# Kernel optimization log

Hardware: AMD Instinct MI355X
Metric: run time of the kernel (lower is better)

## Reference

```python
import jax, jax.numpy as jnp
import numpy as np
import math

B, N, G, H, D = 16, 10000, 100, 128, 2
TANH_CLIP = 10.0
NEG_BIG = -1e8


def setup_inputs() -> dict:
    key = jax.random.key(0)
    ks = jax.random.split(key, 8)
    embeddings = jax.random.normal(ks[0], (B, N, H), dtype=jnp.float32)
    coordinates = jax.random.uniform(ks[1], (B, N, D), dtype=jnp.float32)
    last_node = jax.random.randint(ks[2], (B, G), 0, N)
    # group_ninf_mask: -inf where node already visited, 0 otherwise
    visited = jax.random.bernoulli(ks[3], 0.3, (B, G, N))
    group_ninf_mask = jnp.where(visited, -jnp.inf, 0.0).astype(jnp.float32)
    s = 1.0 / math.sqrt(H)
    Wq_graph_w = jax.random.normal(ks[4], (H, H), dtype=jnp.float32) * s
    Wq_first_w = jax.random.normal(ks[5], (H, H), dtype=jnp.float32) * s
    Wq_last_w = jax.random.normal(ks[6], (H, H), dtype=jnp.float32) * s
    W_visited_w = jax.random.normal(ks[7], (H, H), dtype=jnp.float32) * s
    return {
        "embeddings": embeddings,
        "coordinates": coordinates,
        "last_node": last_node,
        "group_ninf_mask": group_ninf_mask,
        "Wq_graph_w": Wq_graph_w,
        "Wq_first_w": Wq_first_w,
        "Wq_last_w": Wq_last_w,
        "W_visited_w": W_visited_w,
        "S": 0,
    }


def reference(embeddings, coordinates, last_node, group_ninf_mask,
              Wq_graph_w, Wq_first_w, Wq_last_w, W_visited_w, S):
    # --- state built in reset() ---
    # q_graph: Wq_graph(mean over nodes) -> [B,1,H]
    q_graph = jnp.einsum("bnh,oh->bno", jnp.mean(embeddings, axis=1, keepdims=True), Wq_graph_w)
    # logit_k is embeddings^T (multi_pointer == 1 path)

    # --- forward step ---
    # gather last-node embedding: [B,G,H]
    last_emb = jnp.take_along_axis(embeddings, last_node[:, :, None], axis=1)
    q_last = jnp.einsum("bgh,oh->bgo", last_emb, Wq_last_w)
    # q_first is None at the first step -> computed from the same last node
    q_first = jnp.einsum("bgh,oh->bgo", last_emb, Wq_first_w)

    # visited aggregation: mask with -inf -> 1.0, then bmm with embeddings / N
    mask_visited = jnp.where(jnp.isneginf(group_ninf_mask), 1.0, group_ninf_mask)
    agg = jnp.einsum("bgn,bnh->bgh", mask_visited, embeddings) / N
    q_visited = jnp.einsum("bgh,oh->bgo", agg, W_visited_w)

    # distances from last node to every node: cdist -> [B,G,N]
    last_coord = jnp.take_along_axis(coordinates, last_node[:, :, None], axis=1)  # [B,G,D]
    diff = last_coord[:, :, None, :] - coordinates[:, None, :, :]  # [B,G,N,D]
    distances = jnp.sqrt(jnp.maximum(jnp.sum(diff * diff, axis=-1), 1e-12))

    final_q = q_last + q_first + q_graph + q_visited  # add_more_query=True
    score = jnp.einsum("bgh,bnh->bgn", final_q, embeddings) / math.sqrt(H) \
            - distances / math.sqrt(2.0)
    score_clipped = TANH_CLIP * jnp.tanh(score)
    mask_prob = jnp.where(jnp.isneginf(group_ninf_mask), NEG_BIG, group_ninf_mask)
    probs = jax.nn.softmax(score_clipped + mask_prob, axis=-1)
    return probs
```

## Files before the change

### kernel.cpp

```cpp
#include <hip/hip_runtime.h>
#include <math.h>

#define Bc 16
#define Nc 10000
#define Gc 100
#define Hc 128
#define GPAD 104
#define NW 314
#define NTILE 64
#define NTILES 157
#define NSPLIT 32

#define RSH 0.08838834764831845f
#define RS2 0.7071067811865476f

__global__ __launch_bounds__(256, 2)
void k_agg(const float* __restrict__ emb, const float* __restrict__ mask,
           float* __restrict__ agg, unsigned* __restrict__ bmask) {
  __shared__ float se[NTILE][Hc];
  __shared__ float mT[NTILE][108];
  const int b = blockIdx.x;
  const int s = blockIdx.y;
  const int t = threadIdx.x;
  const int tx = t & 15;
  const int ty = t >> 4;
  const int h0 = tx * 8;
  int g0c[2];
  g0c[0] = 4 * ty;
  g0c[1] = 4 * ty + 64;
  if (g0c[1] > 100) g0c[1] = 100;

  float acc[2][4][8];
  #pragma unroll
  for (int p = 0; p < 2; ++p)
    #pragma unroll
    for (int a = 0; a < 4; ++a)
      #pragma unroll
      for (int c = 0; c < 8; ++c) acc[p][a][c] = 0.f;

  const float* eb = emb + (size_t)b * Nc * Hc;
  const float* mb = mask + (size_t)b * Gc * Nc;

  for (int tile = s; tile < NTILES; tile += NSPLIT) {
    const int n0 = tile * NTILE;
    int valid = Nc - n0; if (valid > NTILE) valid = NTILE;
    __syncthreads();
    {
      const float4* src = (const float4*)(eb + (size_t)n0 * Hc);
      float4* dst = (float4*)(&se[0][0]);
      const int validF4 = valid * (Hc / 4);
      #pragma unroll
      for (int k = 0; k < 8; ++k) {
        int idx = k * 256 + t;
        float4 v = {0.f, 0.f, 0.f, 0.f};
        if (idx < validF4) v = src[idx];
        dst[idx] = v;
      }
    }
    #pragma unroll
    for (int k = 0; k < 26; ++k) {
      int lin = k * 256 + t;
      int g = lin >> 6;
      int n = lin & 63;
      float m = 0.f;
      if (n < valid) {
        if (g < Gc) {
          float v = mb[(size_t)g * Nc + n0 + n];
          m = (v < -1e30f) ? 1.0f : v;
        } else if (g == Gc) {
          m = 1.0f;
        }
      }
      mT[n][g] = m;
    }
    __syncthreads();
    if (t < 200) {
      int g = t >> 1, w = t & 1;
      unsigned bits = 0u;
      #pragma unroll
      for (int j = 0; j < 32; ++j)
        if (mT[w * 32 + j][g] != 0.f) bits |= (1u << j);
      bmask[((size_t)b * Gc + g) * NW + 2 * tile + w] = bits;
    }
    #pragma unroll 2
    for (int n = 0; n < NTILE; ++n) {
      float4 e0 = *(const float4*)(&se[n][h0]);
      float4 e1 = *(const float4*)(&se[n][h0 + 4]);
      float ef[8] = {e0.x, e0.y, e0.z, e0.w, e1.x, e1.y, e1.z, e1.w};
      #pragma unroll
      for (int p = 0; p < 2; ++p) {
        float4 mv = *(const float4*)(&mT[n][g0c[p]]);
        float m4[4] = {mv.x, mv.y, mv.z, mv.w};
        #pragma unroll
        for (int a = 0; a < 4; ++a)
          #pragma unroll
          for (int c = 0; c < 8; ++c)
            acc[p][a][c] += m4[a] * ef[c];
      }
    }
  }
  #pragma unroll
  for (int p = 0; p < 2; ++p) {
    #pragma unroll
    for (int a = 0; a < 4; ++a) {
      int g = 4 * ty + 64 * p + a;
      if (g < GPAD) {
        #pragma unroll
        for (int c = 0; c < 8; ++c)
          atomicAdd(&agg[((size_t)b * GPAD + g) * Hc + h0 + c], acc[p][a][c]);
      }
    }
  }
}

__global__ __launch_bounds__(256)
void k_fq(const float* __restrict__ emb, const float* __restrict__ coords,
          const int* __restrict__ last, const float* __restrict__ Wg,
          const float* __restrict__ Wf, const float* __restrict__ Wl,
          const float* __restrict__ Wv, const float* __restrict__ agg,
          float* __restrict__ fq, float* __restrict__ lastc) {
  __shared__ float xt[16][385];
  __shared__ float wT[16][132];
  __shared__ int ln_s[16];
  const int t = threadIdx.x;
  const int row0 = blockIdx.x * 16;

  if (t < 16) {
    int row = row0 + t;
    int b = row / Gc, g = row - b * Gc;
    ln_s[t] = last[b * Gc + g];
  }
  __syncthreads();
  const float invN = 1.0f / (float)Nc;
  #pragma unroll
  for (int k = 0; k < 24; ++k) {
    int lin = k * 256 + t;
    int r = lin / 384, c = lin - r * 384;
    int row = row0 + r;
    int b = row / Gc, g = row - b * Gc;
    float v;
    if (c < 128)       v = emb[((size_t)b * Nc + ln_s[r]) * Hc + c];
    else if (c < 256)  v = agg[((size_t)b * GPAD + g) * Hc + (c - 128)] * invN;
    else               v = agg[((size_t)b * GPAD + Gc) * Hc + (c - 256)] * invN;
    xt[r][c] = v;
  }
  if (t < 32) {
    int r = t >> 1, d = t & 1;
    int row = row0 + r;
    int b = row / Gc;
    lastc[(size_t)row * 2 + d] = coords[((size_t)b * Nc + ln_s[r]) * 2 + d];
  }

  const int tx = t & 31, ty = t >> 5;
  float acc[2][4] = {{0.f,0.f,0.f,0.f},{0.f,0.f,0.f,0.f}};
  for (int kc = 0; kc < 24; ++kc) {
    __syncthreads();
    {
      int j = t & 15, oo = t >> 4;
      int col = kc * 16 + j;
      #pragma unroll
      for (int i = 0; i < 8; ++i) {
        int o = i * 16 + oo;
        float w;
        if (col < 128)      w = Wl[o * Hc + col] + Wf[o * Hc + col];
        else if (col < 256) w = Wv[o * Hc + (col - 128)];
        else                w = Wg[o * Hc + (col - 256)];
        wT[j][o] = w;
      }
    }
    __syncthreads();
    #pragma unroll
    for (int j = 0; j < 16; ++j) {
      int col = kc * 16 + j;
      float x0 = xt[2 * ty][col];
      float x1 = xt[2 * ty + 1][col];
      float4 w = *(const float4*)(&wT[j][4 * tx]);
      float w4[4] = {w.x, w.y, w.z, w.w};
      #pragma unroll
      for (int cc = 0; cc < 4; ++cc) {
        acc[0][cc] += x0 * w4[cc];
        acc[1][cc] += x1 * w4[cc];
      }
    }
  }
  #pragma unroll
  for (int rr = 0; rr < 2; ++rr) {
    int row = row0 + 2 * ty + rr;
    #pragma unroll
    for (int cc = 0; cc < 4; ++cc)
      fq[(size_t)row * Hc + 4 * tx + cc] = acc[rr][cc];
  }
}

__global__ __launch_bounds__(256, 2)
void k_score(const float* __restrict__ emb, const float* __restrict__ coords,
             const float* __restrict__ fq, const float* __restrict__ lastc,
             const unsigned* __restrict__ bmask, float* __restrict__ sums,
             float* __restrict__ out) {
  __shared__ float q_l[52][130];
  __shared__ float eT[Hc][68];
  __shared__ float cxs[NTILE], cys[NTILE];
  __shared__ float lcx[52], lcy[52];
  __shared__ unsigned bm[52][2];
  const int tile = blockIdx.x;
  const int gh = blockIdx.y;
  const int b = blockIdx.z;
  const int t = threadIdx.x;
  const int n0 = tile * NTILE;
  int valid = Nc - n0; if (valid > NTILE) valid = NTILE;

  #pragma unroll
  for (int k = 0; k < 26; ++k) {
    int lin = k * 256 + t;
    int g = lin >> 7, h = lin & 127;
    float v = 0.f;
    if (g < 50) v = fq[((size_t)b * Gc + gh * 50 + g) * Hc + h];
    q_l[g][h] = v;
  }
  {
    const float* ebp = emb + ((size_t)b * Nc + n0) * Hc;
    #pragma unroll
    for (int k = 0; k < 32; ++k) {
      int lin = k * 256 + t;
      int n = lin >> 7, h = lin & 127;
      int col = n ^ (8 * (h & 7));
      eT[h][col] = (n < valid) ? ebp[lin] : 0.f;
    }
  }
  if (t < NTILE) {
    float vx = 0.f, vy = 0.f;
    if (t < valid) {
      vx = coords[((size_t)b * Nc + n0 + t) * 2 + 0];
      vy = coords[((size_t)b * Nc + n0 + t) * 2 + 1];
    }
    cxs[t] = vx; cys[t] = vy;
  }
  if (t < 104) {
    int g = t >> 1, d = t & 1;
    float v = 0.f;
    if (g < 50) v = lastc[((size_t)b * Gc + gh * 50 + g) * 2 + d];
    if (d == 0) lcx[g] = v; else lcy[g] = v;
  }
  if (t >= 104 && t < 208) {
    int u = t - 104;
    int g = u >> 1, w = u & 1;
    unsigned bits = 0u;
    if (g < 50) bits = bmask[((size_t)b * Gc + gh * 50 + g) * NW + 2 * tile + w];
    bm[g][w] = bits;
  }
  __syncthreads();

  const int tx = t & 15, ty = t >> 4;
  const float* qr[4];
  #pragma unroll
  for (int i = 0; i < 4; ++i) {
    int g = ty + 16 * i; if (g > 51) g = 51;
    qr[i] = &q_l[g][0];
  }
  int offs[8];
  #pragma unroll
  for (int c = 0; c < 8; ++c) offs[c] = 4 * (tx ^ (2 * c));

  float acc[4][4];
  #pragma unroll
  for (int i = 0; i < 4; ++i)
    #pragma unroll
    for (int j = 0; j < 4; ++j) acc[i][j] = 0.f;

  for (int hb = 0; hb < Hc; hb += 8) {
    #pragma unroll
    for (int c = 0; c < 8; c += 2) {
      const int h = hb + c;
      float4 ea  = *(const float4*)(&eT[h][offs[c]]);
      float4 ebv = *(const float4*)(&eT[h + 1][offs[c + 1]]);
      float e0[4] = {ea.x, ea.y, ea.z, ea.w};
      float e1[4] = {ebv.x, ebv.y, ebv.z, ebv.w};
      #pragma unroll
      for (int i = 0; i < 4; ++i) {
        float2 qv = *(const float2*)(qr[i] + h);
        #pragma unroll
        for (int j = 0; j < 4; ++j)
          acc[i][j] += qv.x * e0[j] + qv.y * e1[j];
      }
    }
  }
  __syncthreads();
  float* ew = &q_l[0][0];

  #pragma unroll
  for (int i = 0; i < 4; ++i) {
    int g = ty + 16 * i;
    bool gv = (g < 50);
    int gc = g > 51 ? 51 : g;
    float lx = lcx[gc], ly = lcy[gc];
    unsigned b0 = bm[gc][0], b1 = bm[gc][1];
    float ps = 0.f;
    #pragma unroll
    for (int j = 0; j < 4; ++j) {
      int n = 4 * tx + j;
      float dx = lx - cxs[n], dy = ly - cys[n];
      float dist = sqrtf(fmaxf(dx * dx + dy * dy, 1e-12f));
      float sc = acc[i][j] * RSH - dist * RS2;
      sc = fminf(fmaxf(sc, -15.f), 15.f);
      float ex2 = __expf(2.f * sc);
      float th = (ex2 - 1.f) / (ex2 + 1.f);
      float logit = 10.f * th;
      unsigned wb = (n < 32) ? b0 : b1;
      bool vis = ((wb >> (n & 31)) & 1u) != 0u;
      float e = (gv && !vis && (n0 + n) < Nc) ? __expf(logit) : 0.f;
      ps += e;
      ew[g * 65 + n] = e;
    }
    #pragma unroll
    for (int m = 8; m >= 1; m >>= 1) ps += __shfl_xor(ps, m, 64);
    if (tx == 0 && gv) atomicAdd(&sums[b * Gc + gh * 50 + g], ps);
  }
  __syncthreads();
  #pragma unroll
  for (int k = 0; k < 4; ++k) {
    int lin4 = k * 256 + t;
    if (lin4 < 800) {
      int g = lin4 >> 4, n = (lin4 & 15) * 4;
      if (n0 + n < Nc) {
        float4 v;
        v.x = ew[g * 65 + n + 0];
        v.y = ew[g * 65 + n + 1];
        v.z = ew[g * 65 + n + 2];
        v.w = ew[g * 65 + n + 3];
        *(float4*)(&out[((size_t)b * Gc + gh * 50 + g) * Nc + n0 + n]) = v;
      }
    }
  }
}

__global__ __launch_bounds__(256)
void k_norm(float* __restrict__ out, const float* __restrict__ sums) {
  const int i = blockIdx.x * 256 + threadIdx.x;
  float4* o4 = (float4*)out;
  int row = i / 2500;
  float inv = 1.0f / sums[row];
  float4 v = o4[i];
  v.x *= inv; v.y *= inv; v.z *= inv; v.w *= inv;
  o4[i] = v;
}

extern "C" void kernel_launch(void* const* d_in, const int* in_sizes, int n_in,
                              void* d_out, int out_size, void* d_ws, size_t ws_size,
                              hipStream_t stream) {
  const float* emb    = (const float*)d_in[0];
  const float* coords = (const float*)d_in[1];
  const int*   last   = (const int*)d_in[2];
  const float* mask   = (const float*)d_in[3];
  const float* Wg     = (const float*)d_in[4];
  const float* Wf     = (const float*)d_in[5];
  const float* Wl     = (const float*)d_in[6];
  const float* Wv     = (const float*)d_in[7];
  float* out = (float*)d_out;

  float* agg   = (float*)d_ws;
  float* sums  = agg + (size_t)Bc * GPAD * Hc;
  float* fq    = sums + Bc * Gc;
  float* lastc = fq + (size_t)Bc * Gc * Hc;
  unsigned* bmask = (unsigned*)(lastc + (size_t)Bc * Gc * 2);

  size_t zeroBytes = ((size_t)Bc * GPAD * Hc + (size_t)Bc * Gc) * sizeof(float);
  hipMemsetAsync(d_ws, 0, zeroBytes, stream);

  k_agg  <<<dim3(Bc, NSPLIT), 256, 0, stream>>>(emb, mask, agg, bmask);
  k_fq   <<<dim3(100),        256, 0, stream>>>(emb, coords, last, Wg, Wf, Wl, Wv,
                                                agg, fq, lastc);
  k_score<<<dim3(NTILES, 2, Bc), 256, 0, stream>>>(emb, coords, fq, lastc, bmask,
                                                   sums, out);
  k_norm <<<dim3(15625),      256, 0, stream>>>(out, sums);
}
```

Baseline: 754.8 us.

## Use bf16 MFMA split-precision in agg kernel and persistent-tile score kernel

The aggregation GEMM moves from FP32 FMAs to bf16 32x32x16 MFMA. Embeddings are split into hi and lo bf16 parts to keep near-FP32 accuracy, and the visited bitmask is now built with a wave ballot. Per-split partials go to a workspace and are reduced by a new kernel when space allows, otherwise atomics are used. The score kernel now loops over node tiles with 512 threads and 16 splits per batch, writing outputs directly and accumulating row sums in registers to cut atomics and launch count. The risk is lower occupancy and fewer blocks in the score kernel, plus reduced precision on the 0/1 mask operand.

```diff
diff --git a/kernel.cpp b/kernel.cpp
--- a/kernel.cpp
+++ b/kernel.cpp
@@ -4,113 +4,128 @@
 #define Bc 16
 #define Nc 10000
 #define Gc 100
+#define GR 104
 #define Hc 128
-#define GPAD 104
-#define NW 314
 #define NTILE 64
 #define NTILES 157
 #define NSPLIT 32
+#define SSPLIT 16
+#define NWQ 157
 
 #define RSH 0.08838834764831845f
 #define RS2 0.7071067811865476f
 
-__global__ __launch_bounds__(256, 2)
+typedef short bf16x8 __attribute__((ext_vector_type(8)));
+typedef float f32x16 __attribute__((ext_vector_type(16)));
+
+__device__ __forceinline__ unsigned short bf16_rne(float f) {
+  unsigned u = __float_as_uint(f);
+  return (unsigned short)((u + 0x7FFF + ((u >> 16) & 1)) >> 16);
+}
+
+__global__ __launch_bounds__(512, 2)
 void k_agg(const float* __restrict__ emb, const float* __restrict__ mask,
-           float* __restrict__ agg, unsigned* __restrict__ bmask) {
-  __shared__ float se[NTILE][Hc];
-  __shared__ float mT[NTILE][108];
-  const int b = blockIdx.x;
-  const int s = blockIdx.y;
-  const int t = threadIdx.x;
-  const int tx = t & 15;
-  const int ty = t >> 4;
-  const int h0 = tx * 8;
-  int g0c[2];
-  g0c[0] = 4 * ty;
-  g0c[1] = 4 * ty + 64;
-  if (g0c[1] > 100) g0c[1] = 100;
-
-  float acc[2][4][8];
-  #pragma unroll
-  for (int p = 0; p < 2; ++p)
-    #pragma unroll
-    for (int a = 0; a < 4; ++a)
-      #pragma unroll
-      for (int c = 0; c < 8; ++c) acc[p][a][c] = 0.f;
+           float* __restrict__ agg, float* __restrict__ part,
+           unsigned long long* __restrict__ bmq, int useAtomic) {
+  __shared__ unsigned short Am[128 * 64];
+  __shared__ unsigned short Bh[128 * 64];
+  __shared__ unsigned short Bl[128 * 64];
+  const int b = blockIdx.x, s = blockIdx.y, t = threadIdx.x;
+  const int w = t >> 6, l = t & 63;
+  const int rowblk = w & 3;
+  const int colpair = w >> 2;
+
+  if (t < 768) ((int*)&Am[104 * 64])[t] = 0;
+
+  f32x16 acc0, acc1;
+  #pragma unroll
+  for (int i = 0; i < 16; ++i) { acc0[i] = 0.f; acc1[i] = 0.f; }
 
   const float* eb = emb + (size_t)b * Nc * Hc;
   const float* mb = mask + (size_t)b * Gc * Nc;
 
   for (int tile = s; tile < NTILES; tile += NSPLIT) {
     const int n0 = tile * NTILE;
-    int valid = Nc - n0; if (valid > NTILE) valid = NTILE;
-    __syncthreads();
-    {
-      const float4* src = (const float4*)(eb + (size_t)n0 * Hc);
-      float4* dst = (float4*)(&se[0][0]);
-      const int validF4 = valid * (Hc / 4);
-      #pragma unroll
-      for (int k = 0; k < 8; ++k) {
-        int idx = k * 256 + t;
-        float4 v = {0.f, 0.f, 0.f, 0.f};
-        if (idx < validF4) v = src[idx];
-        dst[idx] = v;
-      }
-    }
-    #pragma unroll
-    for (int k = 0; k < 26; ++k) {
-      int lin = k * 256 + t;
-      int g = lin >> 6;
-      int n = lin & 63;
+    const int valid = min(NTILE, Nc - n0);
+    __syncthreads();
+    #pragma unroll
+    for (int k = 0; k < 13; ++k) {
+      int g = k * 8 + w;
+      int n = l;
       float m = 0.f;
-      if (n < valid) {
-        if (g < Gc) {
+      if (g < Gc) {
+        if (n < valid) {
           float v = mb[(size_t)g * Nc + n0 + n];
           m = (v < -1e30f) ? 1.0f : v;
-        } else if (g == Gc) {
-          m = 1.0f;
         }
-      }
-      mT[n][g] = m;
-    }
-    __syncthreads();
-    if (t < 200) {
-      int g = t >> 1, w = t & 1;
-      unsigned bits = 0u;
-      #pragma unroll
-      for (int j = 0; j < 32; ++j)
-        if (mT[w * 32 + j][g] != 0.f) bits |= (1u << j);
-      bmask[((size_t)b * Gc + g) * NW + 2 * tile + w] = bits;
-    }
-    #pragma unroll 2
-    for (int n = 0; n < NTILE; ++n) {
-      float4 e0 = *(const float4*)(&se[n][h0]);
-      float4 e1 = *(const float4*)(&se[n][h0 + 4]);
-      float ef[8] = {e0.x, e0.y, e0.z, e0.w, e1.x, e1.y, e1.z, e1.w};
-      #pragma unroll
-      for (int p = 0; p < 2; ++p) {
-        float4 mv = *(const float4*)(&mT[n][g0c[p]]);
-        float m4[4] = {mv.x, mv.y, mv.z, mv.w};
-        #pragma unroll
-        for (int a = 0; a < 4; ++a)
-          #pragma unroll
-          for (int c = 0; c < 8; ++c)
-            acc[p][a][c] += m4[a] * ef[c];
-      }
-    }
-  }
-  #pragma unroll
-  for (int p = 0; p < 2; ++p) {
-    #pragma unroll
-    for (int a = 0; a < 4; ++a) {
-      int g = 4 * ty + 64 * p + a;
-      if (g < GPAD) {
-        #pragma unroll
-        for (int c = 0; c < 8; ++c)
-          atomicAdd(&agg[((size_t)b * GPAD + g) * Hc + h0 + c], acc[p][a][c]);
-      }
-    }
-  }
+        unsigned long long bits = __ballot(m != 0.f);
+        if (l == 0) bmq[((size_t)b * Gc + g) * NWQ + tile] = bits;
+      } else if (g == Gc) {
+        m = (n < valid) ? 1.0f : 0.f;
+      }
+      int p = (n & 7) | ((((n >> 3) ^ (g & 7))) << 3);
+      Am[g * 64 + p] = bf16_rne(m);
+    }
+    #pragma unroll
+    for (int k = 0; k < 8; ++k) {
+      int lin = k * 512 + t;
+      int n2 = lin >> 7, h = lin & 127;
+      int n = 2 * n2;
+      float v0 = 0.f, v1 = 0.f;
+      if (n < valid)     v0 = eb[(size_t)(n0 + n) * Hc + h];
+      if (n + 1 < valid) v1 = eb[(size_t)(n0 + n + 1) * Hc + h];
+      unsigned short h0 = bf16_rne(v0), h1 = bf16_rne(v1);
+      float r0 = v0 - __uint_as_float((unsigned)h0 << 16);
+      float r1 = v1 - __uint_as_float((unsigned)h1 << 16);
+      unsigned short l0 = bf16_rne(r0), l1 = bf16_rne(r1);
+      int p = (n & 7) | ((((n >> 3) ^ (h & 7))) << 3);
+      *(ushort2*)&Bh[h * 64 + p] = make_ushort2(h0, h1);
+      *(ushort2*)&Bl[h * 64 + p] = make_ushort2(l0, l1);
+    }
+    __syncthreads();
+    #pragma unroll
+    for (int ks = 0; ks < 4; ++ks) {
+      const int n8 = ks * 16 + (l >> 5) * 8;
+      const int ga = rowblk * 32 + (l & 31);
+      const int h0a = colpair * 64 + (l & 31);
+      const int h1a = h0a + 32;
+      bf16x8 af  = *(const bf16x8*)&Am[ga * 64 + (((n8 >> 3) ^ (ga & 7)) << 3)];
+      bf16x8 bh0 = *(const bf16x8*)&Bh[h0a * 64 + (((n8 >> 3) ^ (h0a & 7)) << 3)];
+      bf16x8 bl0 = *(const bf16x8*)&Bl[h0a * 64 + (((n8 >> 3) ^ (h0a & 7)) << 3)];
+      bf16x8 bh1 = *(const bf16x8*)&Bh[h1a * 64 + (((n8 >> 3) ^ (h1a & 7)) << 3)];
+      bf16x8 bl1 = *(const bf16x8*)&Bl[h1a * 64 + (((n8 >> 3) ^ (h1a & 7)) << 3)];
+      acc0 = __builtin_amdgcn_mfma_f32_32x32x16_bf16(af, bh0, acc0, 0, 0, 0);
+      acc0 = __builtin_amdgcn_mfma_f32_32x32x16_bf16(af, bl0, acc0, 0, 0, 0);
+      acc1 = __builtin_amdgcn_mfma_f32_32x32x16_bf16(af, bh1, acc1, 0, 0, 0);
+      acc1 = __builtin_amdgcn_mfma_f32_32x32x16_bf16(af, bl1, acc1, 0, 0, 0);
+    }
+  }
+  const int gbase = rowblk * 32;
+  const int h0a = colpair * 64 + (l & 31);
+  #pragma unroll
+  for (int r = 0; r < 16; ++r) {
+    int g = gbase + (r & 3) + 8 * (r >> 2) + 4 * (l >> 5);
+    if (g < GR) {
+      if (useAtomic) {
+        atomicAdd(&agg[((size_t)b * GR + g) * Hc + h0a],      acc0[r]);
+        atomicAdd(&agg[((size_t)b * GR + g) * Hc + h0a + 32], acc1[r]);
+      } else {
+        float* pp = part + (((size_t)s * Bc + b) * GR + g) * Hc;
+        pp[h0a]      = acc0[r];
+        pp[h0a + 32] = acc1[r];
+      }
+    }
+  }
+}
+
+__global__ __launch_bounds__(256)
+void k_red(const float* __restrict__ part, float* __restrict__ agg) {
+  const int o = blockIdx.x * 256 + threadIdx.x;
+  float sum = 0.f;
+  #pragma unroll
+  for (int s = 0; s < NSPLIT; ++s)
+    sum += part[(size_t)s * Bc * GR * Hc + o];
+  agg[o] = sum;
 }
 
 __global__ __launch_bounds__(256)
@@ -140,8 +155,8 @@
     int b = row / Gc, g = row - b * Gc;
     float v;
     if (c < 128)       v = emb[((size_t)b * Nc + ln_s[r]) * Hc + c];
-    else if (c < 256)  v = agg[((size_t)b * GPAD + g) * Hc + (c - 128)] * invN;
-    else               v = agg[((size_t)b * GPAD + Gc) * Hc + (c - 256)] * invN;
+    else if (c < 256)  v = agg[((size_t)b * GR + g) * Hc + (c - 128)] * invN;
+    else               v = agg[((size_t)b * GR + Gc) * Hc + (c - 256)] * invN;
     xt[r][c] = v;
   }
   if (t < 32) {
@@ -161,11 +176,11 @@
       #pragma unroll
       for (int i = 0; i < 8; ++i) {
         int o = i * 16 + oo;
-        float w;
-        if (col < 128)      w = Wl[o * Hc + col] + Wf[o * Hc + col];
-        else if (col < 256) w = Wv[o * Hc + (col - 128)];
-        else                w = Wg[o * Hc + (col - 256)];
-        wT[j][o] = w;
+        float wv;
+        if (col < 128)      wv = Wl[o * Hc + col] + Wf[o * Hc + col];
+        else if (col < 256) wv = Wv[o * Hc + (col - 128)];
+        else                wv = Wg[o * Hc + (col - 256)];
+        wT[j][o] = wv;
       }
     }
     __syncthreads();
@@ -174,8 +189,8 @@
       int col = kc * 16 + j;
       float x0 = xt[2 * ty][col];
       float x1 = xt[2 * ty + 1][col];
-      float4 w = *(const float4*)(&wT[j][4 * tx]);
-      float w4[4] = {w.x, w.y, w.z, w.w};
+      float4 wv = *(const float4*)(&wT[j][4 * tx]);
+      float w4[4] = {wv.x, wv.y, wv.z, wv.w};
       #pragma unroll
       for (int cc = 0; cc < 4; ++cc) {
         acc[0][cc] += x0 * w4[cc];
@@ -192,48 +207,31 @@
   }
 }
 
-__global__ __launch_bounds__(256, 2)
+__global__ __launch_bounds__(512, 4)
 void k_score(const float* __restrict__ emb, const float* __restrict__ coords,
              const float* __restrict__ fq, const float* __restrict__ lastc,
-             const unsigned* __restrict__ bmask, float* __restrict__ sums,
+             const unsigned* __restrict__ bmw, float* __restrict__ sums,
              float* __restrict__ out) {
   __shared__ float q_l[52][130];
   __shared__ float eT[Hc][68];
   __shared__ float cxs[NTILE], cys[NTILE];
   __shared__ float lcx[52], lcy[52];
-  __shared__ unsigned bm[52][2];
-  const int tile = blockIdx.x;
+  __shared__ unsigned bmt[104];
+  const int s2 = blockIdx.x;
   const int gh = blockIdx.y;
-  const int b = blockIdx.z;
+  const int b  = blockIdx.z;
   const int t = threadIdx.x;
-  const int n0 = tile * NTILE;
-  int valid = Nc - n0; if (valid > NTILE) valid = NTILE;
-
-  #pragma unroll
-  for (int k = 0; k < 26; ++k) {
-    int lin = k * 256 + t;
+  const int tx = t & 31;
+  const int ty = t >> 5;
+  const int l  = t & 63;
+
+  #pragma unroll
+  for (int k = 0; k < 13; ++k) {
+    int lin = k * 512 + t;
     int g = lin >> 7, h = lin & 127;
     float v = 0.f;
     if (g < 50) v = fq[((size_t)b * Gc + gh * 50 + g) * Hc + h];
     q_l[g][h] = v;
-  }
-  {
-    const float* ebp = emb + ((size_t)b * Nc + n0) * Hc;
-    #pragma unroll
-    for (int k = 0; k < 32; ++k) {
-      int lin = k * 256 + t;
-      int n = lin >> 7, h = lin & 127;
-      int col = n ^ (8 * (h & 7));
-      eT[h][col] = (n < valid) ? ebp[lin] : 0.f;
-    }
-  }
-  if (t < NTILE) {
-    float vx = 0.f, vy = 0.f;
-    if (t < valid) {
-      vx = coords[((size_t)b * Nc + n0 + t) * 2 + 0];
-      vy = coords[((size_t)b * Nc + n0 + t) * 2 + 1];
-    }
-    cxs[t] = vx; cys[t] = vy;
   }
   if (t < 104) {
     int g = t >> 1, d = t & 1;
@@ -241,95 +239,99 @@
     if (g < 50) v = lastc[((size_t)b * Gc + gh * 50 + g) * 2 + d];
     if (d == 0) lcx[g] = v; else lcy[g] = v;
   }
-  if (t >= 104 && t < 208) {
-    int u = t - 104;
-    int g = u >> 1, w = u & 1;
-    unsigned bits = 0u;
-    if (g < 50) bits = bmask[((size_t)b * Gc + gh * 50 + g) * NW + 2 * tile + w];
-    bm[g][w] = bits;
-  }
-  __syncthreads();
-
-  const int tx = t & 15, ty = t >> 4;
   const float* qr[4];
   #pragma unroll
   for (int i = 0; i < 4; ++i) {
     int g = ty + 16 * i; if (g > 51) g = 51;
     qr[i] = &q_l[g][0];
   }
-  int offs[8];
-  #pragma unroll
-  for (int c = 0; c < 8; ++c) offs[c] = 4 * (tx ^ (2 * c));
-
-  float acc[4][4];
-  #pragma unroll
-  for (int i = 0; i < 4; ++i)
-    #pragma unroll
-    for (int j = 0; j < 4; ++j) acc[i][j] = 0.f;
-
-  for (int hb = 0; hb < Hc; hb += 8) {
-    #pragma unroll
-    for (int c = 0; c < 8; c += 2) {
-      const int h = hb + c;
-      float4 ea  = *(const float4*)(&eT[h][offs[c]]);
-      float4 ebv = *(const float4*)(&eT[h + 1][offs[c + 1]]);
-      float e0[4] = {ea.x, ea.y, ea.z, ea.w};
-      float e1[4] = {ebv.x, ebv.y, ebv.z, ebv.w};
-      #pragma unroll
-      for (int i = 0; i < 4; ++i) {
-        float2 qv = *(const float2*)(qr[i] + h);
+  float rs[4] = {0.f, 0.f, 0.f, 0.f};
+
+  for (int tile = s2; tile < NTILES; tile += SSPLIT) {
+    const int n0 = tile * NTILE;
+    const int valid = min(NTILE, Nc - n0);
+    __syncthreads();
+    {
+      const float* ebp = emb + ((size_t)b * Nc + n0) * Hc;
+      #pragma unroll
+      for (int k = 0; k < 16; ++k) {
+        int lin = k * 512 + t;
+        int n = lin >> 7, h = lin & 127;
+        int col = n ^ (8 * (h & 7));
+        eT[h][col] = (n < valid) ? ebp[lin] : 0.f;
+      }
+    }
+    if (t < NTILE) {
+      float vx = 0.f, vy = 0.f;
+      if (t < valid) {
+        vx = coords[((size_t)b * Nc + n0 + t) * 2 + 0];
+        vy = coords[((size_t)b * Nc + n0 + t) * 2 + 1];
+      }
+      cxs[t] = vx; cys[t] = vy;
+    }
+    if (t < 100) {
+      int g = t >> 1, ww = t & 1;
+      bmt[t] = bmw[(((size_t)b * Gc + gh * 50 + g) * NWQ + tile) * 2 + ww];
+    }
+    __syncthreads();
+
+    float acc[4][2];
+    #pragma unroll
+    for (int i = 0; i < 4; ++i) { acc[i][0] = 0.f; acc[i][1] = 0.f; }
+
+    for (int hb = 0; hb < Hc; hb += 8) {
+      #pragma unroll
+      for (int c = 0; c < 8; c += 2) {
+        const int h = hb + c;
+        float2 ea  = *(const float2*)(&eT[h][(2 * tx) ^ (8 * c)]);
+        float2 eb2 = *(const float2*)(&eT[h + 1][(2 * tx) ^ (8 * (c + 1))]);
         #pragma unroll
-        for (int j = 0; j < 4; ++j)
-          acc[i][j] += qv.x * e0[j] + qv.y * e1[j];
-      }
-    }
-  }
-  __syncthreads();
-  float* ew = &q_l[0][0];
-
+        for (int i = 0; i < 4; ++i) {
+          float2 qv = *(const float2*)(qr[i] + h);
+          acc[i][0] += qv.x * ea.x + qv.y * eb2.x;
+          acc[i][1] += qv.x * ea.y + qv.y * eb2.y;
+        }
+      }
+    }
+
+    #pragma unroll
+    for (int i = 0; i < 4; ++i) {
+      int g = ty + 16 * i;
+      bool gv = (g < 50);
+      int gc = g > 51 ? 51 : g;
+      float lx = lcx[gc], ly = lcy[gc];
+      unsigned bb0 = gv ? bmt[2 * gc] : 0u, bb1 = gv ? bmt[2 * gc + 1] : 0u;
+      float ps = 0.f;
+      float ev0 = 0.f, ev1 = 0.f;
+      #pragma unroll
+      for (int j = 0; j < 2; ++j) {
+        int n = 2 * tx + j;
+        float dx = lx - cxs[n], dy = ly - cys[n];
+        float dist = sqrtf(fmaxf(dx * dx + dy * dy, 1e-12f));
+        float sc = acc[i][j] * RSH - dist * RS2;
+        sc = fminf(fmaxf(sc, -15.f), 15.f);
+        float ex2 = __expf(2.f * sc);
+        float th = (ex2 - 1.f) / (ex2 + 1.f);
+        float logit = 10.f * th;
+        unsigned wb = (n < 32) ? bb0 : bb1;
+        bool vis = ((wb >> (n & 31)) & 1u) != 0u;
+        float e = (gv && !vis && (n0 + n) < Nc) ? __expf(logit) : 0.f;
+        ps += e;
+        if (j == 0) ev0 = e; else ev1 = e;
+      }
+      if (gv && 2 * tx < valid)
+        *(float2*)&out[((size_t)b * Gc + gh * 50 + g) * Nc + n0 + 2 * tx] =
+            make_float2(ev0, ev1);
+      #pragma unroll
+      for (int m = 1; m <= 16; m <<= 1) ps += __shfl_xor(ps, m, 64);
+      rs[i] += ps;
+    }
+  }
   #pragma unroll
   for (int i = 0; i < 4; ++i) {
     int g = ty + 16 * i;
-    bool gv = (g < 50);
-    int gc = g > 51 ? 51 : g;
-    float lx = lcx[gc], ly = lcy[gc];
-    unsigned b0 = bm[gc][0], b1 = bm[gc][1];
-    float ps = 0.f;
-    #pragma unroll
-    for (int j = 0; j < 4; ++j) {
-      int n = 4 * tx + j;
-      float dx = lx - cxs[n], dy = ly - cys[n];
-      float dist = sqrtf(fmaxf(dx * dx + dy * dy, 1e-12f));
-      float sc = acc[i][j] * RSH - dist * RS2;
-      sc = fminf(fmaxf(sc, -15.f), 15.f);
-      float ex2 = __expf(2.f * sc);
-      float th = (ex2 - 1.f) / (ex2 + 1.f);
-      float logit = 10.f * th;
-      unsigned wb = (n < 32) ? b0 : b1;
-      bool vis = ((wb >> (n & 31)) & 1u) != 0u;
-      float e = (gv && !vis && (n0 + n) < Nc) ? __expf(logit) : 0.f;
-      ps += e;
-      ew[g * 65 + n] = e;
-    }
-    #pragma unroll
-    for (int m = 8; m >= 1; m >>= 1) ps += __shfl_xor(ps, m, 64);
-    if (tx == 0 && gv) atomicAdd(&sums[b * Gc + gh * 50 + g], ps);
-  }
-  __syncthreads();
-  #pragma unroll
-  for (int k = 0; k < 4; ++k) {
-    int lin4 = k * 256 + t;
-    if (lin4 < 800) {
-      int g = lin4 >> 4, n = (lin4 & 15) * 4;
-      if (n0 + n < Nc) {
-        float4 v;
-        v.x = ew[g * 65 + n + 0];
-        v.y = ew[g * 65 + n + 1];
-        v.z = ew[g * 65 + n + 2];
-        v.w = ew[g * 65 + n + 3];
-        *(float4*)(&out[((size_t)b * Gc + gh * 50 + g) * Nc + n0 + n]) = v;
-      }
-    }
+    if ((l & 31) == 0 && g < 50)
+      atomicAdd(&sums[b * Gc + gh * 50 + g], rs[i]);
   }
 }
 
@@ -358,18 +360,22 @@
   float* out = (float*)d_out;
 
   float* agg   = (float*)d_ws;
-  float* sums  = agg + (size_t)Bc * GPAD * Hc;
+  float* sums  = agg + (size_t)Bc * GR * Hc;
   float* fq    = sums + Bc * Gc;
   float* lastc = fq + (size_t)Bc * Gc * Hc;
-  unsigned* bmask = (unsigned*)(lastc + (size_t)Bc * Gc * 2);
-
-  size_t zeroBytes = ((size_t)Bc * GPAD * Hc + (size_t)Bc * Gc) * sizeof(float);
-  hipMemsetAsync(d_ws, 0, zeroBytes, stream);
-
-  k_agg  <<<dim3(Bc, NSPLIT), 256, 0, stream>>>(emb, mask, agg, bmask);
-  k_fq   <<<dim3(100),        256, 0, stream>>>(emb, coords, last, Wg, Wf, Wl, Wv,
-                                                agg, fq, lastc);
-  k_score<<<dim3(NTILES, 2, Bc), 256, 0, stream>>>(emb, coords, fq, lastc, bmask,
-                                                   sums, out);
-  k_norm <<<dim3(15625),      256, 0, stream>>>(out, sums);
-}
+  unsigned long long* bmq = (unsigned long long*)(lastc + (size_t)Bc * Gc * 2);
+  float* part = (float*)(bmq + (size_t)Bc * Gc * NWQ);
+  size_t baseBytes = (size_t)((char*)part - (char*)d_ws);
+  size_t partBytes = (size_t)NSPLIT * Bc * GR * Hc * sizeof(float);
+  int useAtomic = (baseBytes + partBytes > ws_size) ? 1 : 0;
+
+  hipMemsetAsync(d_ws, 0, ((size_t)Bc * GR * Hc + Bc * Gc) * sizeof(float), stream);
+
+  k_agg<<<dim3(Bc, NSPLIT), 512, 0, stream>>>(emb, mask, agg, part, bmq, useAtomic);
+  if (!useAtomic)
+    k_red<<<(Bc * GR * Hc) / 256, 256, 0, stream>>>(part, agg);
+  k_fq<<<100, 256, 0, stream>>>(emb, coords, last, Wg, Wf, Wl, Wv, agg, fq, lastc);
+  k_score<<<dim3(SSPLIT, 2, Bc), 512, 0, stream>>>(emb, coords, fq, lastc,
+                                                   (const unsigned*)bmq, sums, out);
+  k_norm<<<15625, 256, 0, stream>>>(out, sums);
+}
```

Result: faster. 618.1 us (-18.1%).
